# Kernel optimization log

Hardware: AMD Instinct MI355X
Metric: run time of the kernel (lower is better)

## Reference

```python
import jax, jax.numpy as jnp
import numpy as np

B, S, D = 1, 4096, 2048
H, KV, HD = 16, 4, 128
ROPE_BASE = 10000.0


def setup_inputs() -> dict:
    key = jax.random.key(0)
    ks = jax.random.split(key, 5)
    hidden_states = jax.random.normal(ks[0], (B, S, D), dtype=jnp.float32) * 0.02
    Wq = jax.random.normal(ks[1], (D, H * HD), dtype=jnp.float32) * (D ** -0.5)
    Wk = jax.random.normal(ks[2], (D, KV * HD), dtype=jnp.float32) * (D ** -0.5)
    Wv = jax.random.normal(ks[3], (D, KV * HD), dtype=jnp.float32) * (D ** -0.5)
    Wo = jax.random.normal(ks[4], (H * HD, D), dtype=jnp.float32) * ((H * HD) ** -0.5)
    # causal additive mask [1,1,S,S]
    neg = jnp.float32(-1e9)
    causal = jnp.tril(jnp.ones((S, S), dtype=bool))
    attention_mask = jnp.where(causal, 0.0, neg)[None, None, :, :].astype(jnp.float32)
    position_ids = jnp.arange(S, dtype=jnp.int32)[None, :]
    return {"hidden_states": hidden_states, "Wq": Wq, "Wk": Wk, "Wv": Wv,
            "Wo": Wo, "attention_mask": attention_mask, "position_ids": position_ids}


def _rotate_half(x):
    x1, x2 = jnp.split(x, 2, axis=-1)
    return jnp.concatenate([-x2, x1], axis=-1)


def _rope_cos_sin(position_ids):
    # position_ids: [B, S] -> cos/sin [B, 1, S, HD]
    inv_freq = 1.0 / (ROPE_BASE ** (jnp.arange(0, HD, 2, dtype=jnp.float32) / HD))
    freqs = position_ids.astype(jnp.float32)[..., None] * inv_freq  # [B,S,HD/2]
    emb = jnp.concatenate([freqs, freqs], axis=-1)                   # [B,S,HD]
    return jnp.cos(emb)[:, None, :, :], jnp.sin(emb)[:, None, :, :]


def reference(hidden_states, Wq, Wk, Wv, Wo, attention_mask, position_ids):
    bsz, q_len, _ = hidden_states.shape
    # QKV projections -> [B, heads, S, HD]
    q = (hidden_states @ Wq).reshape(bsz, q_len, H, HD).transpose(0, 2, 1, 3)
    k = (hidden_states @ Wk).reshape(bsz, q_len, KV, HD).transpose(0, 2, 1, 3)
    v = (hidden_states @ Wv).reshape(bsz, q_len, KV, HD).transpose(0, 2, 1, 3)
    # inline RoPE
    cos, sin = _rope_cos_sin(position_ids)
    q = q * cos + _rotate_half(q) * sin
    k = k * cos + _rotate_half(k) * sin
    # GQA repeat_interleave on head dim
    rep = H // KV
    k = jnp.repeat(k, rep, axis=1)
    v = jnp.repeat(v, rep, axis=1)
    # attention
    scale = HD ** -0.5
    scores = jnp.einsum('bhqd,bhkd->bhqk', q, k) * scale + attention_mask
    probs = jax.nn.softmax(scores, axis=-1)
    out = jnp.einsum('bhqk,bhkd->bhqd', probs, v)
    out = out.transpose(0, 2, 1, 3).reshape(bsz, q_len, H * HD)
    return out @ Wo
```

## Files before the change

kernel.cpp:

```cpp
#include <hip/hip_runtime.h>
#include <hip/hip_bf16.h>
#include <cstdint>
#include <cmath>

#define S_LEN 4096
#define DMODEL 2048
#define NH 16
#define NKV 4
#define HD 128
#define NQKV 3072

typedef unsigned short u16;
typedef unsigned int u32;
typedef __attribute__((ext_vector_type(8))) __bf16 bf16x8;
typedef __attribute__((ext_vector_type(4))) float f32x4;
typedef __attribute__((ext_vector_type(16))) float f32x16;
typedef __attribute__((ext_vector_type(4))) int i32x4;

__device__ __forceinline__ u16 f2bf(float f) {
  __bf16 h = (__bf16)f;
  return __builtin_bit_cast(u16, h);
}
__device__ __forceinline__ float bf2f(u16 u) {
  return (float)__builtin_bit_cast(__bf16, u);
}
__device__ __forceinline__ u32 pk2(float a, float b) {
  return (u32)f2bf(a) | ((u32)f2bf(b) << 16);
}

__device__ __forceinline__ void gload16(const void* g, void* l) {
  __builtin_amdgcn_global_load_lds(
      (const __attribute__((address_space(1))) void*)g,
      (__attribute__((address_space(3))) void*)l, 16, 0, 0);
}

__global__ void k_f32_to_bf16(const float* __restrict__ src, u16* __restrict__ dst, int n4) {
  int i = blockIdx.x * blockDim.x + threadIdx.x;
  if (i < n4) {
    float4 v = reinterpret_cast<const float4*>(src)[i];
    ushort4 o = make_ushort4(f2bf(v.x), f2bf(v.y), f2bf(v.z), f2bf(v.w));
    reinterpret_cast<ushort4*>(dst)[i] = o;
  }
}

__global__ void k_transpose_f32_bf16(const float* __restrict__ src, int srcStride,
                                     u16* __restrict__ dst, int dstStride) {
  __shared__ float tile[32][33];
  int n0 = blockIdx.x * 32, k0 = blockIdx.y * 32;
  int tx = threadIdx.x, ty = threadIdx.y;
#pragma unroll
  for (int r = 0; r < 32; r += 8)
    tile[ty + r][tx] = src[(size_t)(k0 + ty + r) * srcStride + n0 + tx];
  __syncthreads();
#pragma unroll
  for (int r = 0; r < 32; r += 8)
    dst[(size_t)(n0 + ty + r) * dstStride + k0 + tx] = f2bf(tile[tx][ty + r]);
}

__global__ void k_transpose_bf16(const u16* __restrict__ src, int srcStride,
                                 u16* __restrict__ dst, int dstStride) {
  __shared__ u16 tile[32][33];
  int n0 = blockIdx.x * 32, k0 = blockIdx.y * 32;
  int tx = threadIdx.x, ty = threadIdx.y;
#pragma unroll
  for (int r = 0; r < 32; r += 8)
    tile[ty + r][tx] = src[(size_t)(k0 + ty + r) * srcStride + n0 + tx];
  __syncthreads();
#pragma unroll
  for (int r = 0; r < 32; r += 8)
    dst[(size_t)(n0 + ty + r) * dstStride + k0 + tx] = tile[tx][ty + r];
}

__global__ void k_rope_tab(const int* __restrict__ pos_ids, float2* __restrict__ tab) {
  int idx = blockIdx.x * blockDim.x + threadIdx.x;
  int s = idx >> 6, dh = idx & 63;
  const float L2B = 13.287712379549449f;
  float pos = (float)pos_ids[s];
  float invf = exp2f(-(float)dh * (L2B / 64.0f));
  float ang = pos * invf;
  tab[idx] = make_float2(cosf(ang), sinf(ang));
}

__global__ void k_rope(const u16* __restrict__ qkv, const float2* __restrict__ tab,
                       u16* __restrict__ Qb, u16* __restrict__ Kb) {
  int s = blockIdx.x;
  const u16* row = qkv + (size_t)s * NQKV;
  const float QSCALE = 0.08838834764831845f * 1.4426950408889634f;
  for (int c = threadIdx.x; c < DMODEL + NKV * HD; c += blockDim.x) {
    int d = c & 127;
    int dh = d & 63;
    float2 cs = tab[s * 64 + dh];
    float x = bf2f(row[c]);
    float xp = bf2f(row[c ^ 64]);
    float rot = (d < 64) ? -xp : xp;
    float out = x * cs.x + rot * cs.y;
    if (c < DMODEL) {
      int h = c >> 7;
      out *= QSCALE;
      Qb[((size_t)h * S_LEN + s) * HD + d] = f2bf(out);
    } else {
      int kvh = (c - DMODEL) >> 7;
      Kb[((size_t)kvh * S_LEN + s) * HD + d] = f2bf(out);
    }
  }
}

template <int OUT_BF16>
__global__ __launch_bounds__(256) void k_gemm_bt(const u16* __restrict__ A,
                                                 const u16* __restrict__ BT,
                                                 void* __restrict__ C, int M, int N, int K) {
  __shared__ __align__(16) u16 As[128 * 32];
  __shared__ __align__(16) u16 Bs[128 * 32];
  const int tid = threadIdx.x, wave = tid >> 6, lane = tid & 63;
  const int fr = lane & 15, fq = lane >> 4;
  const int rowBase = blockIdx.y * 128, colBase = blockIdx.x * 128;
  const int wr = wave >> 1, wc = wave & 1;
  f32x4 acc[4][4] = {};
  const int nk = K >> 5;
  for (int kt = 0; kt < nk; ++kt) {
    const int k0 = kt << 5;
#pragma unroll
    for (int p = 0; p < 2; ++p) {
      int cbase = p * 256 + wave * 64;
      int chunk = cbase + lane;
      int r = chunk >> 2, cb = chunk & 3;
      gload16(A + (size_t)(rowBase + r) * K + k0 + cb * 8, (char*)As + cbase * 16);
      gload16(BT + (size_t)(colBase + r) * K + k0 + cb * 8, (char*)Bs + cbase * 16);
    }
    __syncthreads();
    bf16x8 a[4], b[4];
#pragma unroll
    for (int m = 0; m < 4; ++m)
      a[m] = *reinterpret_cast<const bf16x8*>(&As[(wr * 64 + m * 16 + fr) * 32 + fq * 8]);
#pragma unroll
    for (int n = 0; n < 4; ++n)
      b[n] = *reinterpret_cast<const bf16x8*>(&Bs[(wc * 64 + n * 16 + fr) * 32 + fq * 8]);
#pragma unroll
    for (int m = 0; m < 4; ++m)
#pragma unroll
      for (int n = 0; n < 4; ++n)
        acc[m][n] = __builtin_amdgcn_mfma_f32_16x16x32_bf16(a[m], b[n], acc[m][n], 0, 0, 0);
    __syncthreads();
  }
#pragma unroll
  for (int m = 0; m < 4; ++m) {
    int row0 = rowBase + wr * 64 + m * 16 + fq * 4;
#pragma unroll
    for (int n = 0; n < 4; ++n) {
      int col = colBase + wc * 64 + n * 16 + fr;
#pragma unroll
      for (int j = 0; j < 4; ++j) {
        if (OUT_BF16)
          ((u16*)C)[(size_t)(row0 + j) * N + col] = f2bf(acc[m][n][j]);
        else
          ((float*)C)[(size_t)(row0 + j) * N + col] = acc[m][n][j];
      }
    }
  }
}

__device__ __forceinline__ void stage_kv128(const u16* __restrict__ Kbk,
                                            const u16* __restrict__ VTk, int kb,
                                            char* KsB, char* VsB, int tid) {
#pragma unroll
  for (int it = 0; it < 4; ++it) {
    int slot = it * 512 + tid;
    int r = slot >> 4, cb = slot & 15;
    int cbs = cb ^ (r & 15);
    gload16(Kbk + (size_t)(kb + r) * HD + cbs * 8, KsB + slot * 16);
    gload16(VTk + (size_t)r * S_LEN + kb + cbs * 8, VsB + slot * 16);
  }
}

__global__ __launch_bounds__(512, 2) void k_attn(const u16* __restrict__ Qb,
                                                 const u16* __restrict__ Kb,
                                                 const u16* __restrict__ VT,
                                                 u16* __restrict__ AO) {
  __shared__ __align__(16) u16 Ks[2][128 * 128];
  __shared__ __align__(16) u16 Vs[2][128 * 128];
  const int h = blockIdx.x;
  const int p = blockIdx.y;
  const int kv = h >> 2;
  const int tid = threadIdx.x, wave = tid >> 6, lane = tid & 63;
  const int grp = wave >> 2, pr = wave & 3;
  const int ql = lane & 31, hi = lane >> 5;
  const float DEFER_THR = 11.541560327111707f;

  const u16* Kbk = Kb + (size_t)kv * S_LEN * HD;
  const u16* VTk = VT + (size_t)kv * HD * S_LEN;

#pragma unroll 1
  for (int half = 0; half < 2; ++half) {
    const int qt = half ? p : (31 - p);
    const int qg0w = qt * 128 + pr * 32;
    const int qglob = qg0w + ql;

    __syncthreads();
    stage_kv128(Kbk, VTk, 0, (char*)Ks[0], (char*)Vs[0], tid);

    bf16x8 qf[8];
    {
      const u16* qp = Qb + ((size_t)h * S_LEN + qglob) * HD;
#pragma unroll
      for (int t = 0; t < 8; ++t)
        qf[t] = *reinterpret_cast<const bf16x8*>(qp + t * 16 + hi * 8);
    }
    f32x16 o[4] = {};
    float m = -INFINITY, l = 0.f;

    __syncthreads();

    int buf = 0;
    const int nkt = qt + 1;
    for (int kt = 0; kt < nkt; ++kt) {
      if (kt + 1 < nkt)
        stage_kv128(Kbk, VTk, (kt + 1) * 128, (char*)Ks[buf ^ 1], (char*)Vs[buf ^ 1], tid);
      const int kbg = kt * 128 + grp * 64;
      if (kbg <= qg0w + 31) {
        const char* Kc = (const char*)Ks[buf];
        const char* Vc = (const char*)Vs[buf];

        f32x16 st0 = {}, st1 = {};
#pragma unroll
        for (int t = 0; t < 8; ++t) {
          int ch = (2 * t + hi) ^ (ql & 15);
          const int r0 = grp * 64 + ql, r1 = grp * 64 + 32 + ql;
          bf16x8 kf0 = *reinterpret_cast<const bf16x8*>(Kc + r0 * 256 + ch * 16);
          bf16x8 kf1 = *reinterpret_cast<const bf16x8*>(Kc + r1 * 256 + ch * 16);
          st0 = __builtin_amdgcn_mfma_f32_32x32x16_bf16(kf0, qf[t], st0, 0, 0, 0);
          st1 = __builtin_amdgcn_mfma_f32_32x32x16_bf16(kf1, qf[t], st1, 0, 0, 0);
        }
        if (kbg + 63 > qg0w) {
#pragma unroll
          for (int r = 0; r < 16; ++r) {
            int kl = (r & 3) + 8 * (r >> 2) + 4 * hi;
            if (kbg + kl > qglob) st0[r] = -1e30f;
            if (kbg + 32 + kl > qglob) st1[r] = -1e30f;
          }
        }
        float mx[16];
#pragma unroll
        for (int r = 0; r < 16; ++r) mx[r] = fmaxf(st0[r], st1[r]);
#pragma unroll
        for (int s = 8; s > 0; s >>= 1)
#pragma unroll
          for (int r = 0; r < 16; ++r)
            if (r < s) mx[r] = fmaxf(mx[r], mx[r + s]);
        float tmax = fmaxf(mx[0], __shfl_xor(mx[0], 32));
        if (__any(tmax - m > DEFER_THR)) {
          float mn = fmaxf(m, tmax);
          float corr = exp2f(m - mn);
          m = mn;
          l *= corr;
#pragma unroll
          for (int d0 = 0; d0 < 4; ++d0) o[d0] *= corr;
        }
        float sm[16];
#pragma unroll
        for (int r = 0; r < 16; ++r) {
          st0[r] = exp2f(st0[r] - m);
          st1[r] = exp2f(st1[r] - m);
          sm[r] = st0[r] + st1[r];
        }
#pragma unroll
        for (int s = 8; s > 0; s >>= 1)
#pragma unroll
          for (int r = 0; r < 16; ++r)
            if (r < s) sm[r] += sm[r + s];
        l += sm[0] + __shfl_xor(sm[0], 32);

        bf16x8 pa[4];
#pragma unroll
        for (int kc = 0; kc < 4; ++kc) {
          int rb = 8 * (kc & 1);
          u32 w0, w1, w2, w3;
          if (kc < 2) {
            w0 = pk2(st0[rb + 0], st0[rb + 1]);
            w1 = pk2(st0[rb + 2], st0[rb + 3]);
            w2 = pk2(st0[rb + 4], st0[rb + 5]);
            w3 = pk2(st0[rb + 6], st0[rb + 7]);
          } else {
            w0 = pk2(st1[rb + 0], st1[rb + 1]);
            w1 = pk2(st1[rb + 2], st1[rb + 3]);
            w2 = pk2(st1[rb + 4], st1[rb + 5]);
            w3 = pk2(st1[rb + 6], st1[rb + 7]);
          }
          u32 xw0 = (u32)__shfl_xor((int)w0, 32);
          u32 xw1 = (u32)__shfl_xor((int)w1, 32);
          u32 xw2 = (u32)__shfl_xor((int)w2, 32);
          u32 xw3 = (u32)__shfl_xor((int)w3, 32);
          i32x4 pw;
          pw[0] = (int)(hi ? xw2 : w0);
          pw[1] = (int)(hi ? xw3 : w1);
          pw[2] = (int)(hi ? w2 : xw0);
          pw[3] = (int)(hi ? w3 : xw1);
          pa[kc] = __builtin_bit_cast(bf16x8, pw);
        }
#pragma unroll
        for (int d0 = 0; d0 < 4; ++d0) {
          int dr = d0 * 32 + ql;
#pragma unroll
          for (int kc = 0; kc < 4; ++kc) {
            int ch = (grp * 8 + 2 * kc + hi) ^ (ql & 15);
            bf16x8 vf = *reinterpret_cast<const bf16x8*>(Vc + dr * 256 + ch * 16);
            o[d0] = __builtin_amdgcn_mfma_f32_32x32x16_bf16(vf, pa[kc], o[d0], 0, 0, 0);
          }
        }
      }
      __syncthreads();
      buf ^= 1;
    }

    float2* exch = (float2*)Ks;
    float2* mlb = (float2*)Vs;
    if (grp == 0) {
#pragma unroll
      for (int rp = 0; rp < 8; ++rp) {
        float2 v2, v3;
        v2.x = o[2][2 * rp]; v2.y = o[2][2 * rp + 1];
        v3.x = o[3][2 * rp]; v3.y = o[3][2 * rp + 1];
        exch[((2 * 8 + rp) * 4 + pr) * 64 + lane] = v2;
        exch[((3 * 8 + rp) * 4 + pr) * 64 + lane] = v3;
      }
    } else {
#pragma unroll
      for (int rp = 0; rp < 8; ++rp) {
        float2 v0, v1;
        v0.x = o[0][2 * rp]; v0.y = o[0][2 * rp + 1];
        v1.x = o[1][2 * rp]; v1.y = o[1][2 * rp + 1];
        exch[((0 * 8 + rp) * 4 + pr) * 64 + lane] = v0;
        exch[((1 * 8 + rp) * 4 + pr) * 64 + lane] = v1;
      }
    }
    if (hi == 0) {
      float2 v;
      v.x = m;
      v.y = l;
      mlb[(grp * 4 + pr) * 32 + ql] = v;
    }
    __syncthreads();
    {
      float2 pml = mlb[((1 - grp) * 4 + pr) * 32 + ql];
      float mm = fmaxf(m, pml.x);
      float fa = exp2f(m - mm), fb = exp2f(pml.x - mm);
      float ll = l * fa + pml.y * fb;
      float inv = 1.0f / ll;
      u16* aoRow = AO + (size_t)qglob * DMODEL + h * HD;
      if (grp == 0) {
#pragma unroll
        for (int rp = 0; rp < 8; ++rp) {
          int r = 2 * rp;
          int dbase = (r & 3) + 8 * (r >> 2) + 4 * hi;
          float2 po0 = exch[((0 * 8 + rp) * 4 + pr) * 64 + lane];
          float u0 = (o[0][r] * fa + po0.x * fb) * inv;
          float u1 = (o[0][r + 1] * fa + po0.y * fb) * inv;
          *reinterpret_cast<u32*>(aoRow + 0 * 32 + dbase) = pk2(u0, u1);
          float2 po1 = exch[((1 * 8 + rp) * 4 + pr) * 64 + lane];
          u0 = (o[1][r] * fa + po1.x * fb) * inv;
          u1 = (o[1][r + 1] * fa + po1.y * fb) * inv;
          *reinterpret_cast<u32*>(aoRow + 1 * 32 + dbase) = pk2(u0, u1);
        }
      } else {
#pragma unroll
        for (int rp = 0; rp < 8; ++rp) {
          int r = 2 * rp;
          int dbase = (r & 3) + 8 * (r >> 2) + 4 * hi;
          float2 po2 = exch[((2 * 8 + rp) * 4 + pr) * 64 + lane];
          float u0 = (o[2][r] * fa + po2.x * fb) * inv;
          float u1 = (o[2][r + 1] * fa + po2.y * fb) * inv;
          *reinterpret_cast<u32*>(aoRow + 2 * 32 + dbase) = pk2(u0, u1);
          float2 po3 = exch[((3 * 8 + rp) * 4 + pr) * 64 + lane];
          u0 = (o[3][r] * fa + po3.x * fb) * inv;
          u1 = (o[3][r + 1] * fa + po3.y * fb) * inv;
          *reinterpret_cast<u32*>(aoRow + 3 * 32 + dbase) = pk2(u0, u1);
        }
      }
    }
  }
}

extern "C" void kernel_launch(void* const* d_in, const int* in_sizes, int n_in,
                              void* d_out, int out_size, void* d_ws, size_t ws_size,
                              hipStream_t stream) {
  const float* hidden = (const float*)d_in[0];
  const float* Wq = (const float*)d_in[1];
  const float* Wk = (const float*)d_in[2];
  const float* Wv = (const float*)d_in[3];
  const float* Wo = (const float*)d_in[4];
  const int* pos_ids = (const int*)d_in[6];
  float* out = (float*)d_out;

  char* ws = (char*)d_ws;
  u16* Xb   = (u16*)(ws);
  u16* Wt   = (u16*)(ws + (16ull << 20));
  u16* WoT  = (u16*)(ws + (28ull << 20));
  u16* QKVb = (u16*)(ws + (36ull << 20));
  u16* Qb   = (u16*)(ws + (60ull << 20));
  u16* Kb   = (u16*)(ws + (76ull << 20));
  u16* VT   = (u16*)(ws + (80ull << 20));
  float2* tab = (float2*)(ws + (82ull << 20));
  u16* AO   = QKVb;

  dim3 tb(32, 8);
  k_f32_to_bf16<<<dim3((S_LEN * DMODEL / 4) / 256), dim3(256), 0, stream>>>(
      hidden, Xb, S_LEN * DMODEL / 4);
  k_transpose_f32_bf16<<<dim3(64, 64), tb, 0, stream>>>(Wq, 2048, Wt, 2048);
  k_transpose_f32_bf16<<<dim3(16, 64), tb, 0, stream>>>(Wk, 512, Wt + (size_t)2048 * 2048, 2048);
  k_transpose_f32_bf16<<<dim3(16, 64), tb, 0, stream>>>(Wv, 512, Wt + (size_t)2560 * 2048, 2048);
  k_transpose_f32_bf16<<<dim3(64, 64), tb, 0, stream>>>(Wo, 2048, WoT, 2048);
  k_rope_tab<<<dim3(S_LEN * 64 / 256), dim3(256), 0, stream>>>(pos_ids, tab);

  k_gemm_bt<1><<<dim3(24, 32), 256, 0, stream>>>(Xb, Wt, QKVb, S_LEN, NQKV, DMODEL);

  k_rope<<<dim3(S_LEN), 256, 0, stream>>>(QKVb, tab, Qb, Kb);
  k_transpose_bf16<<<dim3(16, 128), tb, 0, stream>>>(QKVb + 2560, NQKV, VT, S_LEN);

  k_attn<<<dim3(NH, 16), 512, 0, stream>>>(Qb, Kb, VT, AO);

  k_gemm_bt<0><<<dim3(16, 32), 256, 0, stream>>>(AO, WoT, out, S_LEN, DMODEL, DMODEL);
}
```

Before: 281.4 us.

## Split attention KV range across two blocks and combine partials in a new kernel

The attention kernel now launches a third grid dimension of two and gives each block alternating 64-key tiles, so each block stages half the keys with smaller LDS buffers and a higher occupancy bound. Each split writes an unnormalized bf16 partial output plus its running max and sum to workspace, and a new combine kernel merges the two splits and normalizes. This doubles the number of blocks on the GPU to improve occupancy and load balance for the 256-block causal launch. In exchange it adds an extra launch, partial outputs rounded to bf16 before the merge, extra global traffic, and a reshuffled workspace layout in which buffers are aliased.

```diff
diff --git a/kernel.cpp b/kernel.cpp
--- a/kernel.cpp
+++ b/kernel.cpp
@@ -159,27 +159,37 @@
   }
 }
 
-__device__ __forceinline__ void stage_kv128(const u16* __restrict__ Kbk,
-                                            const u16* __restrict__ VTk, int kb,
-                                            char* KsB, char* VsB, int tid) {
-#pragma unroll
-  for (int it = 0; it < 4; ++it) {
+#define OP_ESTRIDE ((size_t)NH * 32 * 128 * 128)
+
+__device__ __forceinline__ void stage_kv64(const u16* __restrict__ Kbk,
+                                           const u16* __restrict__ VTk, int kb,
+                                           char* KsB, char* VsB, int tid) {
+#pragma unroll
+  for (int it = 0; it < 2; ++it) {
     int slot = it * 512 + tid;
     int r = slot >> 4, cb = slot & 15;
-    int cbs = cb ^ (r & 15);
-    gload16(Kbk + (size_t)(kb + r) * HD + cbs * 8, KsB + slot * 16);
-    gload16(VTk + (size_t)r * S_LEN + kb + cbs * 8, VsB + slot * 16);
-  }
-}
-
-__global__ __launch_bounds__(512, 2) void k_attn(const u16* __restrict__ Qb,
+    gload16(Kbk + (size_t)(kb + r) * HD + (size_t)((cb ^ (r & 15)) * 8), KsB + slot * 16);
+    int d = slot >> 3, vb = slot & 7;
+    gload16(VTk + (size_t)d * S_LEN + kb + (vb ^ (d & 7)) * 8, VsB + slot * 16);
+  }
+}
+
+__device__ __forceinline__ void sl_w(float* p, int off, const f32x16& v) {
+#pragma unroll
+  for (int r = 0; r < 16; r += 4)
+    *reinterpret_cast<float4*>(p + off + r) = make_float4(v[r], v[r + 1], v[r + 2], v[r + 3]);
+}
+
+__global__ __launch_bounds__(512, 4) void k_attn(const u16* __restrict__ Qb,
                                                  const u16* __restrict__ Kb,
                                                  const u16* __restrict__ VT,
-                                                 u16* __restrict__ AO) {
-  __shared__ __align__(16) u16 Ks[2][128 * 128];
-  __shared__ __align__(16) u16 Vs[2][128 * 128];
+                                                 u16* __restrict__ Op,
+                                                 float2* __restrict__ mlG) {
+  __shared__ __align__(16) u16 Ks[2][64 * 128];
+  __shared__ __align__(16) u16 Vs[2][128 * 64];
   const int h = blockIdx.x;
   const int p = blockIdx.y;
+  const int e = blockIdx.z;
   const int kv = h >> 2;
   const int tid = threadIdx.x, wave = tid >> 6, lane = tid & 63;
   const int grp = wave >> 2, pr = wave & 3;
@@ -196,7 +206,7 @@
     const int qglob = qg0w + ql;
 
     __syncthreads();
-    stage_kv128(Kbk, VTk, 0, (char*)Ks[0], (char*)Vs[0], tid);
+    stage_kv64(Kbk, VTk, e * 64, (char*)Ks[0], (char*)Vs[0], tid);
 
     bf16x8 qf[8];
     {
@@ -211,36 +221,33 @@
     __syncthreads();
 
     int buf = 0;
-    const int nkt = qt + 1;
-    for (int kt = 0; kt < nkt; ++kt) {
-      if (kt + 1 < nkt)
-        stage_kv128(Kbk, VTk, (kt + 1) * 128, (char*)Ks[buf ^ 1], (char*)Vs[buf ^ 1], tid);
-      const int kbg = kt * 128 + grp * 64;
+    const int nkt = 2 * qt + 2;
+    for (int kt = e; kt < nkt; kt += 2) {
+      if (kt + 2 < nkt)
+        stage_kv64(Kbk, VTk, (kt + 2) * 64, (char*)Ks[buf ^ 1], (char*)Vs[buf ^ 1], tid);
+      const int kbg = kt * 64 + grp * 32;
       if (kbg <= qg0w + 31) {
         const char* Kc = (const char*)Ks[buf];
         const char* Vc = (const char*)Vs[buf];
 
-        f32x16 st0 = {}, st1 = {};
+        f32x16 st = {};
+        const int r0 = grp * 32 + ql;
 #pragma unroll
         for (int t = 0; t < 8; ++t) {
           int ch = (2 * t + hi) ^ (ql & 15);
-          const int r0 = grp * 64 + ql, r1 = grp * 64 + 32 + ql;
-          bf16x8 kf0 = *reinterpret_cast<const bf16x8*>(Kc + r0 * 256 + ch * 16);
-          bf16x8 kf1 = *reinterpret_cast<const bf16x8*>(Kc + r1 * 256 + ch * 16);
-          st0 = __builtin_amdgcn_mfma_f32_32x32x16_bf16(kf0, qf[t], st0, 0, 0, 0);
-          st1 = __builtin_amdgcn_mfma_f32_32x32x16_bf16(kf1, qf[t], st1, 0, 0, 0);
-        }
-        if (kbg + 63 > qg0w) {
+          bf16x8 kf = *reinterpret_cast<const bf16x8*>(Kc + r0 * 256 + ch * 16);
+          st = __builtin_amdgcn_mfma_f32_32x32x16_bf16(kf, qf[t], st, 0, 0, 0);
+        }
+        if (kbg + 31 > qg0w) {
 #pragma unroll
           for (int r = 0; r < 16; ++r) {
             int kl = (r & 3) + 8 * (r >> 2) + 4 * hi;
-            if (kbg + kl > qglob) st0[r] = -1e30f;
-            if (kbg + 32 + kl > qglob) st1[r] = -1e30f;
+            if (kbg + kl > qglob) st[r] = -1e30f;
           }
         }
         float mx[16];
 #pragma unroll
-        for (int r = 0; r < 16; ++r) mx[r] = fmaxf(st0[r], st1[r]);
+        for (int r = 0; r < 16; ++r) mx[r] = st[r];
 #pragma unroll
         for (int s = 8; s > 0; s >>= 1)
 #pragma unroll
@@ -258,9 +265,8 @@
         float sm[16];
 #pragma unroll
         for (int r = 0; r < 16; ++r) {
-          st0[r] = exp2f(st0[r] - m);
-          st1[r] = exp2f(st1[r] - m);
-          sm[r] = st0[r] + st1[r];
+          st[r] = exp2f(st[r] - m);
+          sm[r] = st[r];
         }
 #pragma unroll
         for (int s = 8; s > 0; s >>= 1)
@@ -269,114 +275,115 @@
             if (r < s) sm[r] += sm[r + s];
         l += sm[0] + __shfl_xor(sm[0], 32);
 
-        bf16x8 pa[4];
-#pragma unroll
-        for (int kc = 0; kc < 4; ++kc) {
-          int rb = 8 * (kc & 1);
-          u32 w0, w1, w2, w3;
-          if (kc < 2) {
-            w0 = pk2(st0[rb + 0], st0[rb + 1]);
-            w1 = pk2(st0[rb + 2], st0[rb + 3]);
-            w2 = pk2(st0[rb + 4], st0[rb + 5]);
-            w3 = pk2(st0[rb + 6], st0[rb + 7]);
-          } else {
-            w0 = pk2(st1[rb + 0], st1[rb + 1]);
-            w1 = pk2(st1[rb + 2], st1[rb + 3]);
-            w2 = pk2(st1[rb + 4], st1[rb + 5]);
-            w3 = pk2(st1[rb + 6], st1[rb + 7]);
-          }
-          u32 xw0 = (u32)__shfl_xor((int)w0, 32);
-          u32 xw1 = (u32)__shfl_xor((int)w1, 32);
-          u32 xw2 = (u32)__shfl_xor((int)w2, 32);
-          u32 xw3 = (u32)__shfl_xor((int)w3, 32);
+        bf16x8 pa0, pa1;
+        {
+          u32 w0 = pk2(st[0], st[1]), w1 = pk2(st[2], st[3]);
+          u32 w2 = pk2(st[4], st[5]), w3 = pk2(st[6], st[7]);
+          u32 xw0 = (u32)__shfl_xor((int)w0, 32), xw1 = (u32)__shfl_xor((int)w1, 32);
+          u32 xw2 = (u32)__shfl_xor((int)w2, 32), xw3 = (u32)__shfl_xor((int)w3, 32);
           i32x4 pw;
           pw[0] = (int)(hi ? xw2 : w0);
           pw[1] = (int)(hi ? xw3 : w1);
           pw[2] = (int)(hi ? w2 : xw0);
           pw[3] = (int)(hi ? w3 : xw1);
-          pa[kc] = __builtin_bit_cast(bf16x8, pw);
+          pa0 = __builtin_bit_cast(bf16x8, pw);
+          w0 = pk2(st[8], st[9]);   w1 = pk2(st[10], st[11]);
+          w2 = pk2(st[12], st[13]); w3 = pk2(st[14], st[15]);
+          xw0 = (u32)__shfl_xor((int)w0, 32); xw1 = (u32)__shfl_xor((int)w1, 32);
+          xw2 = (u32)__shfl_xor((int)w2, 32); xw3 = (u32)__shfl_xor((int)w3, 32);
+          pw[0] = (int)(hi ? xw2 : w0);
+          pw[1] = (int)(hi ? xw3 : w1);
+          pw[2] = (int)(hi ? w2 : xw0);
+          pw[3] = (int)(hi ? w3 : xw1);
+          pa1 = __builtin_bit_cast(bf16x8, pw);
         }
 #pragma unroll
         for (int d0 = 0; d0 < 4; ++d0) {
           int dr = d0 * 32 + ql;
-#pragma unroll
-          for (int kc = 0; kc < 4; ++kc) {
-            int ch = (grp * 8 + 2 * kc + hi) ^ (ql & 15);
-            bf16x8 vf = *reinterpret_cast<const bf16x8*>(Vc + dr * 256 + ch * 16);
-            o[d0] = __builtin_amdgcn_mfma_f32_32x32x16_bf16(vf, pa[kc], o[d0], 0, 0, 0);
-          }
+          int sw = dr & 7;
+          bf16x8 vf0 = *reinterpret_cast<const bf16x8*>(
+              Vc + dr * 128 + ((grp * 4 + 0 + hi) ^ sw) * 16);
+          o[d0] = __builtin_amdgcn_mfma_f32_32x32x16_bf16(vf0, pa0, o[d0], 0, 0, 0);
+          bf16x8 vf1 = *reinterpret_cast<const bf16x8*>(
+              Vc + dr * 128 + ((grp * 4 + 2 + hi) ^ sw) * 16);
+          o[d0] = __builtin_amdgcn_mfma_f32_32x32x16_bf16(vf1, pa1, o[d0], 0, 0, 0);
         }
       }
       __syncthreads();
       buf ^= 1;
     }
 
-    float2* exch = (float2*)Ks;
-    float2* mlb = (float2*)Vs;
+    float2* mlb = (float2*)Ks;
+    if (hi == 0) mlb[(grp * 4 + pr) * 32 + ql] = make_float2(m, l);
+    __syncthreads();
+    float2 pml = mlb[((1 - grp) * 4 + pr) * 32 + ql];
+    float mm = fmaxf(m, pml.x);
+    float fa = (mm > -INFINITY) ? exp2f(m - mm) : 0.f;
+    float fb = (mm > -INFINITY) ? exp2f(pml.x - mm) : 0.f;
+    float ll = l * fa + pml.y * fb;
+    __syncthreads();
+    float* exK = (float*)Ks;
+    float* exV = (float*)Vs;
+    const int off = (pr * 64 + lane) * 16;
     if (grp == 0) {
-#pragma unroll
-      for (int rp = 0; rp < 8; ++rp) {
-        float2 v2, v3;
-        v2.x = o[2][2 * rp]; v2.y = o[2][2 * rp + 1];
-        v3.x = o[3][2 * rp]; v3.y = o[3][2 * rp + 1];
-        exch[((2 * 8 + rp) * 4 + pr) * 64 + lane] = v2;
-        exch[((3 * 8 + rp) * 4 + pr) * 64 + lane] = v3;
-      }
+      sl_w(exK, off, o[2]);
+      sl_w(exK + 4096, off, o[3]);
     } else {
-#pragma unroll
-      for (int rp = 0; rp < 8; ++rp) {
-        float2 v0, v1;
-        v0.x = o[0][2 * rp]; v0.y = o[0][2 * rp + 1];
-        v1.x = o[1][2 * rp]; v1.y = o[1][2 * rp + 1];
-        exch[((0 * 8 + rp) * 4 + pr) * 64 + lane] = v0;
-        exch[((1 * 8 + rp) * 4 + pr) * 64 + lane] = v1;
-      }
-    }
-    if (hi == 0) {
-      float2 v;
-      v.x = m;
-      v.y = l;
-      mlb[(grp * 4 + pr) * 32 + ql] = v;
-    }
+      sl_w(exV, off, o[0]);
+      sl_w(exV + 4096, off, o[1]);
+    }
+    if (grp == 0 && hi == 0)
+      mlG[(((size_t)e * NH + h) * 32 + qt) * 128 + pr * 32 + ql] = make_float2(mm, ll);
     __syncthreads();
     {
-      float2 pml = mlb[((1 - grp) * 4 + pr) * 32 + ql];
-      float mm = fmaxf(m, pml.x);
-      float fa = exp2f(m - mm), fb = exp2f(pml.x - mm);
-      float ll = l * fa + pml.y * fb;
-      float inv = 1.0f / ll;
-      u16* aoRow = AO + (size_t)qglob * DMODEL + h * HD;
+      u16* opRow = Op + (size_t)e * OP_ESTRIDE +
+                   (((size_t)h * 32 + qt) * 128 + pr * 32 + ql) * 128;
       if (grp == 0) {
 #pragma unroll
         for (int rp = 0; rp < 8; ++rp) {
           int r = 2 * rp;
           int dbase = (r & 3) + 8 * (r >> 2) + 4 * hi;
-          float2 po0 = exch[((0 * 8 + rp) * 4 + pr) * 64 + lane];
-          float u0 = (o[0][r] * fa + po0.x * fb) * inv;
-          float u1 = (o[0][r + 1] * fa + po0.y * fb) * inv;
-          *reinterpret_cast<u32*>(aoRow + 0 * 32 + dbase) = pk2(u0, u1);
-          float2 po1 = exch[((1 * 8 + rp) * 4 + pr) * 64 + lane];
-          u0 = (o[1][r] * fa + po1.x * fb) * inv;
-          u1 = (o[1][r + 1] * fa + po1.y * fb) * inv;
-          *reinterpret_cast<u32*>(aoRow + 1 * 32 + dbase) = pk2(u0, u1);
+          float q0a = exV[off + r], q0b = exV[off + r + 1];
+          float q1a = exV[4096 + off + r], q1b = exV[4096 + off + r + 1];
+          *reinterpret_cast<u32*>(opRow + 0 * 32 + dbase) =
+              pk2(o[0][r] * fa + q0a * fb, o[0][r + 1] * fa + q0b * fb);
+          *reinterpret_cast<u32*>(opRow + 1 * 32 + dbase) =
+              pk2(o[1][r] * fa + q1a * fb, o[1][r + 1] * fa + q1b * fb);
         }
       } else {
 #pragma unroll
         for (int rp = 0; rp < 8; ++rp) {
           int r = 2 * rp;
           int dbase = (r & 3) + 8 * (r >> 2) + 4 * hi;
-          float2 po2 = exch[((2 * 8 + rp) * 4 + pr) * 64 + lane];
-          float u0 = (o[2][r] * fa + po2.x * fb) * inv;
-          float u1 = (o[2][r + 1] * fa + po2.y * fb) * inv;
-          *reinterpret_cast<u32*>(aoRow + 2 * 32 + dbase) = pk2(u0, u1);
-          float2 po3 = exch[((3 * 8 + rp) * 4 + pr) * 64 + lane];
-          u0 = (o[3][r] * fa + po3.x * fb) * inv;
-          u1 = (o[3][r + 1] * fa + po3.y * fb) * inv;
-          *reinterpret_cast<u32*>(aoRow + 3 * 32 + dbase) = pk2(u0, u1);
+          float q2a = exK[off + r], q2b = exK[off + r + 1];
+          float q3a = exK[4096 + off + r], q3b = exK[4096 + off + r + 1];
+          *reinterpret_cast<u32*>(opRow + 2 * 32 + dbase) =
+              pk2(o[2][r] * fa + q2a * fb, o[2][r + 1] * fa + q2b * fb);
+          *reinterpret_cast<u32*>(opRow + 3 * 32 + dbase) =
+              pk2(o[3][r] * fa + q3a * fb, o[3][r + 1] * fa + q3b * fb);
         }
       }
     }
   }
+}
+
+__global__ void k_comb(const u16* __restrict__ Op, const float2* __restrict__ mlG,
+                       u16* __restrict__ AO) {
+  int s = blockIdx.x, h = blockIdx.y;
+  int qt = s >> 7, row = s & 127;
+  int t = threadIdx.x;
+  size_t base = (((size_t)h * 32 + qt) * 128 + row) * 128;
+  float2 ml0 = mlG[(((size_t)0 * NH + h) * 32 + qt) * 128 + row];
+  float2 ml1 = mlG[(((size_t)1 * NH + h) * 32 + qt) * 128 + row];
+  float M = fmaxf(ml0.x, ml1.x);
+  float w0 = (ml0.x > -INFINITY) ? exp2f(ml0.x - M) : 0.f;
+  float w1 = (ml1.x > -INFINITY) ? exp2f(ml1.x - M) : 0.f;
+  float inv = 1.0f / (ml0.y * w0 + ml1.y * w1);
+  u32 a = *reinterpret_cast<const u32*>(Op + base + t * 2);
+  u32 b = *reinterpret_cast<const u32*>(Op + OP_ESTRIDE + base + t * 2);
+  float o0 = bf2f((u16)a) * w0 + bf2f((u16)b) * w1;
+  float o1 = bf2f((u16)(a >> 16)) * w0 + bf2f((u16)(b >> 16)) * w1;
+  *reinterpret_cast<u32*>(AO + (size_t)s * DMODEL + h * HD + t * 2) = pk2(o0 * inv, o1 * inv);
 }
 
 extern "C" void kernel_launch(void* const* d_in, const int* in_sizes, int n_in,
@@ -391,15 +398,19 @@
   float* out = (float*)d_out;
 
   char* ws = (char*)d_ws;
-  u16* Xb   = (u16*)(ws);
-  u16* Wt   = (u16*)(ws + (16ull << 20));
-  u16* WoT  = (u16*)(ws + (28ull << 20));
-  u16* QKVb = (u16*)(ws + (36ull << 20));
-  u16* Qb   = (u16*)(ws + (60ull << 20));
-  u16* Kb   = (u16*)(ws + (76ull << 20));
-  u16* VT   = (u16*)(ws + (80ull << 20));
-  float2* tab = (float2*)(ws + (82ull << 20));
-  u16* AO   = QKVb;
+  u16* WoT  = (u16*)(ws);
+  u16* Wt   = (u16*)(ws + (8ull << 20));
+  u16* Qb   = (u16*)(ws + (8ull << 20));
+  u16* Kb   = (u16*)(ws + (24ull << 20));
+  u16* VT   = (u16*)(ws + (28ull << 20));
+  u16* Xb   = (u16*)(ws + (32ull << 20));
+  u16* AO   = (u16*)(ws + (32ull << 20));
+  float2* tab = (float2*)(ws + (48ull << 20));
+  u16* QKVb = (u16*)(ws + (50ull << 20));
+  u16* Op   = (u16*)(ws + (48ull << 20));
+  float2* mlG = (float2*)(ws + (80ull << 20));
+
+  Qb = (u16*)(ws + (8ull << 20));
 
   dim3 tb(32, 8);
   k_f32_to_bf16<<<dim3((S_LEN * DMODEL / 4) / 256), dim3(256), 0, stream>>>(
@@ -415,7 +426,8 @@
   k_rope<<<dim3(S_LEN), 256, 0, stream>>>(QKVb, tab, Qb, Kb);
   k_transpose_bf16<<<dim3(16, 128), tb, 0, stream>>>(QKVb + 2560, NQKV, VT, S_LEN);
 
-  k_attn<<<dim3(NH, 16), 512, 0, stream>>>(Qb, Kb, VT, AO);
+  k_attn<<<dim3(NH, 16, 2), 512, 0, stream>>>(Qb, Kb, VT, Op, mlG);
+  k_comb<<<dim3(S_LEN, NH), 64, 0, stream>>>(Op, mlG, AO);
 
   k_gemm_bt<0><<<dim3(16, 32), 256, 0, stream>>>(AO, WoT, out, S_LEN, DMODEL, DMODEL);
 }
```

Result: slower. 416.2 us (+47.9%).
